# Optimization experiments

Hardware: AMD Instinct MI355X
Metric: run time of the kernel (lower is better)

Reference implementation:

```python
import jax, jax.numpy as jnp
import numpy as np

B, S, D, H = 2, 2048, 1024, 16
HD = D // H          # 64
ROT = HD // 2        # 32

def _rope(x, cos, sin):
    # x: [B,S,H,HD] -> pairs [B,S,H,ROT,2]; cos/sin: [S,ROT] -> [1,S,1,ROT]
    x2 = x.reshape(x.shape[:3] + (ROT, 2))
    x0, x1 = x2[..., 0], x2[..., 1]
    c = cos[None, :, None, :]
    s = sin[None, :, None, :]
    out = jnp.stack([x0 * c - x1 * s, x1 * c + x0 * s], axis=-1)
    return out.reshape(x.shape)

def setup_inputs() -> dict:
    key = jax.random.key(0)
    ks = jax.random.split(key, 5)
    hidden_states = jax.random.normal(ks[0], (B, S, D), dtype=jnp.float32)
    # proper rotary cos/sin table: [S, ROT, 2]
    inv_freq = 1.0 / (10000.0 ** (np.arange(0, ROT, dtype=np.float32) / ROT))
    t = np.arange(S, dtype=np.float32)
    ang = np.outer(t, inv_freq)  # [S, ROT]
    freqs = jnp.asarray(np.stack([np.cos(ang), np.sin(ang)], axis=-1), dtype=jnp.float32)
    sc = 1.0 / np.sqrt(D)
    wq = jax.random.normal(ks[1], (D, D), dtype=jnp.float32) * sc
    wk = jax.random.normal(ks[2], (D, D), dtype=jnp.float32) * sc
    wv = jax.random.normal(ks[3], (D, D), dtype=jnp.float32) * sc
    wo = jax.random.normal(ks[4], (D, D), dtype=jnp.float32) * sc
    return {"hidden_states": hidden_states, "freqs": freqs, "wq": wq, "wk": wk, "wv": wv, "wo": wo}

def reference(hidden_states, freqs, wq, wk, wv, wo):
    b, s, _ = hidden_states.shape
    scaling = HD ** -0.5
    q = (hidden_states @ wq.T).reshape(b, s, H, HD)
    k = (hidden_states @ wk.T).reshape(b, s, H, HD)
    v = (hidden_states @ wv.T).reshape(b, s, H, HD)
    cos, sin = freqs[:s, :, 0], freqs[:s, :, 1]
    q = _rope(q, cos, sin)
    k = _rope(k, cos, sin)
    # [B,H,S,S] scores, fp32 softmax
    scores = jnp.einsum('bqhd,bkhd->bhqk', q, k) * scaling
    attn = jax.nn.softmax(scores.astype(jnp.float32), axis=-1).astype(q.dtype)
    out = jnp.einsum('bhqk,bkhd->bqhd', attn, v).reshape(b, s, D)
    return out @ wo.T
```

## Files before the change

kernel.cpp:

```cpp
#include <hip/hip_runtime.h>
#include <hip/hip_bf16.h>

typedef __attribute__((ext_vector_type(8))) short bf16x8;
typedef __attribute__((ext_vector_type(4))) float f32x4;
typedef __attribute__((ext_vector_type(16))) float f32x16;
typedef __attribute__((ext_vector_type(2))) float f32x2;
typedef unsigned short u16;

#define Bc   2
#define Sc   2048
#define Dc   1024
#define Hc   16
#define HDc  64
#define ROTc 32
#define Mrows 4096

__device__ __forceinline__ u16 f2bf(float x) {
  union { float f; unsigned u; } v{x};
  unsigned r = v.u + 0x7fffu + ((v.u >> 16) & 1u);
  return (u16)(r >> 16);
}
__device__ __forceinline__ float bf2f(u16 x) {
  union { unsigned u; float f; } v{(unsigned)x << 16};
  return v.f;
}
__device__ __forceinline__ unsigned cvtpk(float a, float b) {
  unsigned r;
  asm("v_cvt_pk_bf16_f32 %0, %1, %2" : "=v"(r) : "v"(a), "v"(b));
  return r;
}
__device__ __forceinline__ f32x2 pmax2(f32x2 a, f32x2 b) {
  f32x2 r;
  r.x = fmaxf(a.x, b.x);
  r.y = fmaxf(a.y, b.y);
  return r;
}

__device__ __forceinline__ void gload_lds16(const void* g, void* l) {
  __builtin_amdgcn_global_load_lds(
      (const __attribute__((address_space(1))) void*)g,
      (__attribute__((address_space(3))) void*)l, 16, 0, 0);
}

__global__ void cvt_all(const float* __restrict__ h, const float* __restrict__ q,
                        const float* __restrict__ k, const float* __restrict__ v,
                        const float* __restrict__ o,
                        u16* __restrict__ hb, u16* __restrict__ qb, u16* __restrict__ kb,
                        u16* __restrict__ vb, u16* __restrict__ ob) {
  size_t i = ((size_t)blockIdx.x * 256 + threadIdx.x) * 4;
  const float* s;
  u16* d;
  size_t off;
  if (i < (size_t)Mrows * Dc) {
    s = h; d = hb; off = i;
  } else {
    size_t j = i - (size_t)Mrows * Dc;
    int w = (int)(j >> 20);
    off = j & ((1u << 20) - 1);
    s = (w == 0) ? q : (w == 1) ? k : (w == 2) ? v : o;
    d = (w == 0) ? qb : (w == 1) ? kb : (w == 2) ? vb : ob;
  }
  float4 val = *reinterpret_cast<const float4*>(s + off);
  u16 r0 = f2bf(val.x), r1 = f2bf(val.y), r2 = f2bf(val.z), r3 = f2bf(val.w);
  ushort4 outv = {r0, r1, r2, r3};
  *reinterpret_cast<ushort4*>(d + off) = outv;
}

__global__ void gemm_qkv(const u16* __restrict__ A, const u16* __restrict__ W0,
                         const u16* __restrict__ W1, const u16* __restrict__ W2,
                         const float* __restrict__ freqs,
                         u16* __restrict__ Qo, u16* __restrict__ Ko,
                         u16* __restrict__ Vo) {
  __shared__ u16 As[128 * 32];
  __shared__ u16 Bs[128 * 32];
  const int by = blockIdx.y;
  const int wsel = by >> 3;
  const int n0 = (by & 7) * 128;
  const int m0 = blockIdx.x * 128;
  const u16* Bm = (wsel == 0) ? W0 : (wsel == 1) ? W1 : W2;
  const int t = threadIdx.x;
  const int w = t >> 6;
  const int lane = t & 63;
  const int wm = w >> 1, wn = w & 1;
  const int c = lane & 15, g = lane >> 4;
  const int srow = t >> 2, skoff = (t & 3) * 8;

  f32x4 acc[4][4] = {};

  const u16* ag = A + (size_t)(m0 + srow) * Dc + skoff;
  const u16* bg = Bm + (size_t)(n0 + srow) * Dc + skoff;
  u16* al = &As[(w * 16) * 32];
  u16* bl = &Bs[(w * 16) * 32];

  for (int k0 = 0; k0 < Dc; k0 += 32) {
    gload_lds16(ag + k0, al);
    gload_lds16(ag + k0 + (size_t)64 * Dc, al + 64 * 32);
    gload_lds16(bg + k0, bl);
    gload_lds16(bg + k0 + (size_t)64 * Dc, bl + 64 * 32);
    __syncthreads();
    bf16x8 a[4], b[4];
#pragma unroll
    for (int f = 0; f < 4; ++f) {
      a[f] = *(const bf16x8*)&As[(wm * 64 + f * 16 + c) * 32 + g * 8];
      b[f] = *(const bf16x8*)&Bs[(wn * 64 + f * 16 + c) * 32 + g * 8];
    }
#pragma unroll
    for (int fm = 0; fm < 4; ++fm)
#pragma unroll
      for (int fn = 0; fn < 4; ++fn)
        acc[fm][fn] =
            __builtin_amdgcn_mfma_f32_16x16x32_bf16(a[fm], b[fn], acc[fm][fn], 0, 0, 0);
    __syncthreads();
  }

  u16* dst = (wsel == 0) ? Qo : (wsel == 1) ? Ko : Vo;
  const float qsc = (wsel == 0) ? 0.125f * 1.44269504f : 1.0f;
  const int codd = c & 1;
#pragma unroll
  for (int fm = 0; fm < 4; ++fm)
#pragma unroll
    for (int fn = 0; fn < 4; ++fn)
#pragma unroll
      for (int r = 0; r < 4; ++r) {
        const int m = m0 + wm * 64 + fm * 16 + g * 4 + r;
        const int n = n0 + wn * 64 + fn * 16 + c;
        float v = acc[fm][fn][r];
        const int b = m >> 11, s = m & (Sc - 1);
        const int hh = n >> 6, d = n & 63;
        size_t idx;
        if (wsel < 2) {
          const float other = __shfl_xor(v, 1);
          const float2 f = reinterpret_cast<const float2*>(freqs)[s * ROTc + (d >> 1)];
          v = codd ? (v * f.x + other * f.y) : (v * f.x - other * f.y);
          v *= qsc;
          idx = (((size_t)(b * Hc + hh) * Sc) + s) * HDc + d;
        } else {
          idx = ((size_t)(b * Hc + hh) * HDc + d) * Sc + s;
        }
        dst[idx] = f2bf(v);
      }
}

__global__ void gemm_out(const u16* __restrict__ A, const u16* __restrict__ Bm,
                         float* __restrict__ C) {
  __shared__ u16 As[64 * 32];
  __shared__ u16 Bs[128 * 32];
  const int m0 = blockIdx.x * 64;
  const int n0 = blockIdx.y * 128;
  const int t = threadIdx.x;
  const int w = t >> 6;
  const int lane = t & 63;
  const int wm = w >> 1, wn = w & 1;
  const int c = lane & 15, g = lane >> 4;
  const int srow = t >> 2, skoff = (t & 3) * 8;

  f32x4 acc[2][4] = {};

  const u16* ag = A + (size_t)(m0 + srow) * Dc + skoff;
  const u16* bg = Bm + (size_t)(n0 + srow) * Dc + skoff;
  u16* al = &As[(w * 16) * 32];
  u16* bl = &Bs[(w * 16) * 32];

  for (int k0 = 0; k0 < Dc; k0 += 32) {
    gload_lds16(ag + k0, al);
    gload_lds16(bg + k0, bl);
    gload_lds16(bg + k0 + (size_t)64 * Dc, bl + 64 * 32);
    __syncthreads();
    bf16x8 a[2], b[4];
#pragma unroll
    for (int f = 0; f < 2; ++f)
      a[f] = *(const bf16x8*)&As[(wm * 32 + f * 16 + c) * 32 + g * 8];
#pragma unroll
    for (int f = 0; f < 4; ++f)
      b[f] = *(const bf16x8*)&Bs[(wn * 64 + f * 16 + c) * 32 + g * 8];
#pragma unroll
    for (int fm = 0; fm < 2; ++fm)
#pragma unroll
      for (int fn = 0; fn < 4; ++fn)
        acc[fm][fn] =
            __builtin_amdgcn_mfma_f32_16x16x32_bf16(a[fm], b[fn], acc[fm][fn], 0, 0, 0);
    __syncthreads();
  }

#pragma unroll
  for (int fm = 0; fm < 2; ++fm)
#pragma unroll
    for (int fn = 0; fn < 4; ++fn)
#pragma unroll
      for (int r = 0; r < 4; ++r) {
        const int m = m0 + wm * 32 + fm * 16 + g * 4 + r;
        const int n = n0 + wn * 64 + fn * 16 + c;
        C[(size_t)m * Dc + n] = acc[fm][fn][r];
      }
}

__global__ __launch_bounds__(256, 2) void flash_attn(
    const u16* __restrict__ Q, const u16* __restrict__ Kb,
    const u16* __restrict__ Vt, u16* __restrict__ Ob) {
  __shared__ u16 Ks[2][32 * 128];
  __shared__ u16 Vs[2][32 * 128];
  const int orig = blockIdx.x;
  const int wg = (orig & 7) * 64 + (orig >> 3);
  const int bh = wg >> 4;
  const int q0 = (wg & 15) * 128;
  const int t = threadIdx.x, w = t >> 6, lane = t & 63;
  const int l31 = lane & 31, hi = lane >> 5;
  const int sr = t >> 4;
  const int su = (t & 15) ^ (sr & 15);
  const int skv = sr + ((su >> 3) << 5);
  const int sd8 = (su & 7) * 8;
  const int rsw = (l31 & 15);

  const u16* Qp = Q + (size_t)bh * Sc * HDc;
  const u16* Kp = Kb + (size_t)bh * Sc * HDc;
  const u16* Vp = Vt + (size_t)bh * HDc * Sc;

  const int q = q0 + w * 32 + l31;
  bf16x8 aq[4];
#pragma unroll
  for (int kd = 0; kd < 4; ++kd)
    aq[kd] = *(const bf16x8*)(Qp + (size_t)q * HDc + kd * 16 + hi * 8);

  float m_run = -1e30f, l_run = 0.f;
  f32x16 o0 = {}, o1 = {};
  bf16x8 va0[4], va1[4];

  auto STAGE = [&](int tile, int bb) {
    const int base = tile * 64;
    gload_lds16(Kp + (size_t)(base + skv) * HDc + sd8, &Ks[bb][w * 512]);
    gload_lds16(Kp + (size_t)(base + skv + 16) * HDc + sd8, &Ks[bb][2048 + w * 512]);
    gload_lds16(Vp + (size_t)skv * Sc + base + sd8, &Vs[bb][w * 512]);
    gload_lds16(Vp + (size_t)(skv + 16) * Sc + base + sd8, &Vs[bb][2048 + w * 512]);
  };
  auto QKF = [&](const u16* kbase, f32x16& S0, f32x16& S1) {
    __builtin_amdgcn_s_setprio(1);
#pragma unroll
    for (int kd = 0; kd < 4; ++kd) {
      const int u0 = kd * 2 + hi;
      bf16x8 a0 = *(const bf16x8*)&kbase[l31 * 128 + (u0 ^ rsw) * 8];
      bf16x8 a1 = *(const bf16x8*)&kbase[l31 * 128 + ((u0 + 8) ^ rsw) * 8];
      S0 = __builtin_amdgcn_mfma_f32_32x32x16_bf16(a0, aq[kd], S0, 0, 0, 0);
      S1 = __builtin_amdgcn_mfma_f32_32x32x16_bf16(a1, aq[kd], S1, 0, 0, 0);
    }
    __builtin_amdgcn_s_setprio(0);
  };
  auto LOADV = [&](const u16* vbase) {
#pragma unroll
    for (int ks = 0; ks < 4; ++ks) {
      const int uv = ks * 2 + hi;
      va0[ks] = *(const bf16x8*)&vbase[l31 * 128 + (uv ^ rsw) * 8];
      va1[ks] = *(const bf16x8*)&vbase[l31 * 128 + ((uv + 8) ^ rsw) * 8];
    }
  };
  auto SMPV = [&](f32x16& S0, f32x16& S1) {
    f32x2 t4[4];
#pragma unroll
    for (int i = 0; i < 4; ++i) {
      f32x2 e0; e0.x = S0[2 * i]; e0.y = S0[2 * i + 1];
      f32x2 e1; e1.x = S0[2 * i + 8]; e1.y = S0[2 * i + 9];
      f32x2 e2; e2.x = S1[2 * i]; e2.y = S1[2 * i + 1];
      f32x2 e3; e3.x = S1[2 * i + 8]; e3.y = S1[2 * i + 9];
      t4[i] = pmax2(pmax2(e0, e1), pmax2(e2, e3));
    }
    f32x2 tp = pmax2(pmax2(t4[0], t4[1]), pmax2(t4[2], t4[3]));
    float mt = fmaxf(tp.x, tp.y);
    mt = fmaxf(mt, __shfl_xor(mt, 32));
    const bool skip = __all(mt <= m_run + 8.0f);
    if (!skip) {
      const float mn2 = fmaxf(m_run, mt);
      const float scl = __builtin_amdgcn_exp2f(m_run - mn2);
      m_run = mn2;
      l_run *= scl;
      o0 *= scl;
      o1 *= scl;
    }
    const float mn = m_run;
#pragma unroll
    for (int r = 0; r < 16; ++r) {
      S0[r] = __builtin_amdgcn_exp2f(S0[r] - mn);
      S1[r] = __builtin_amdgcn_exp2f(S1[r] - mn);
    }
    f32x2 ac;
    ac.x = 0.f; ac.y = 0.f;
#pragma unroll
    for (int i = 0; i < 8; ++i) {
      f32x2 e0; e0.x = S0[2 * i]; e0.y = S0[2 * i + 1];
      f32x2 e1; e1.x = S1[2 * i]; e1.y = S1[2 * i + 1];
      ac += e0 + e1;
    }
    float rs = ac.x + ac.y;
    rs += __shfl_xor(rs, 32);
    l_run += rs;
    unsigned pk0[8], pk1[8];
#pragma unroll
    for (int B = 0; B < 4; ++B)
#pragma unroll
      for (int s2 = 0; s2 < 2; ++s2) {
        pk0[B * 2 + s2] = cvtpk(S0[4 * B + 2 * s2], S0[4 * B + 2 * s2 + 1]);
        pk1[B * 2 + s2] = cvtpk(S1[4 * B + 2 * s2], S1[4 * B + 2 * s2 + 1]);
      }
    bf16x8 bpv[4];
#pragma unroll
    for (int ks = 0; ks < 4; ++ks) {
      const unsigned* pk = (ks >> 1) ? pk1 : pk0;
      const int m2 = (ks & 1) * 4;
      const unsigned A0 = pk[m2 + 0], A1 = pk[m2 + 1];
      const unsigned B0 = pk[m2 + 2], B1 = pk[m2 + 3];
      const unsigned L0 = hi ? B0 : A0, L1 = hi ? B1 : A1;
      const unsigned R0 = hi ? A0 : B0, R1 = hi ? A1 : B1;
      const unsigned X0 = __shfl_xor(R0, 32), X1 = __shfl_xor(R1, 32);
      union { unsigned u[4]; bf16x8 v; } bp;
      bp.u[0] = hi ? X0 : L0;
      bp.u[1] = hi ? X1 : L1;
      bp.u[2] = hi ? L0 : X0;
      bp.u[3] = hi ? L1 : X1;
      bpv[ks] = bp.v;
    }
    __builtin_amdgcn_s_setprio(1);
#pragma unroll
    for (int ks = 0; ks < 4; ++ks) {
      o0 = __builtin_amdgcn_mfma_f32_32x32x16_bf16(va0[ks], bpv[ks], o0, 0, 0, 0);
      o1 = __builtin_amdgcn_mfma_f32_32x32x16_bf16(va1[ks], bpv[ks], o1, 0, 0, 0);
    }
    __builtin_amdgcn_s_setprio(0);
  };

  STAGE(0, 0);
  STAGE(1, 1);
  __syncthreads();
  f32x16 sp0 = {}, sp1 = {};
  QKF(&Ks[0][0], sp0, sp1);
  LOADV(&Vs[0][0]);
  __syncthreads();

  int buf = 1;
  for (int tt = 1; tt < 32; ++tt) {
    if (tt < 31) STAGE(tt + 1, buf ^ 1);
    f32x16 sn0 = {}, sn1 = {};
    QKF(&Ks[buf][0], sn0, sn1);
    SMPV(sp0, sp1);
    LOADV(&Vs[buf][0]);
    __syncthreads();
    sp0 = sn0;
    sp1 = sn1;
    buf ^= 1;
  }
  SMPV(sp0, sp1);

  const float rl = 1.0f / l_run;
  const int b = bh >> 4, hh = bh & 15;
  u16* orow = Ob + ((size_t)b * Sc + q) * Dc + hh * HDc;
#pragma unroll
  for (int B2 = 0; B2 < 4; ++B2) {
    const float v0 = o0[4 * B2 + 0] * rl, v1 = o0[4 * B2 + 1] * rl;
    const float v2 = o0[4 * B2 + 2] * rl, v3 = o0[4 * B2 + 3] * rl;
    uint2 pv;
    pv.x = cvtpk(v0, v1);
    pv.y = cvtpk(v2, v3);
    *reinterpret_cast<uint2*>(orow + 8 * B2 + 4 * hi) = pv;
  }
#pragma unroll
  for (int B2 = 0; B2 < 4; ++B2) {
    const float v0 = o1[4 * B2 + 0] * rl, v1 = o1[4 * B2 + 1] * rl;
    const float v2 = o1[4 * B2 + 2] * rl, v3 = o1[4 * B2 + 3] * rl;
    uint2 pv;
    pv.x = cvtpk(v0, v1);
    pv.y = cvtpk(v2, v3);
    *reinterpret_cast<uint2*>(orow + 32 + 8 * B2 + 4 * hi) = pv;
  }
}

extern "C" void kernel_launch(void* const* d_in, const int* in_sizes, int n_in,
                              void* d_out, int out_size, void* d_ws, size_t ws_size,
                              hipStream_t stream) {
  (void)in_sizes; (void)n_in; (void)out_size; (void)ws_size;
  const float* hidden = (const float*)d_in[0];
  const float* freqs = (const float*)d_in[1];
  const float* wq = (const float*)d_in[2];
  const float* wk = (const float*)d_in[3];
  const float* wv = (const float*)d_in[4];
  const float* wo = (const float*)d_in[5];
  float* out = (float*)d_out;

  char* ws = (char*)d_ws;
  const size_t MB8 = (size_t)Mrows * Dc * 2;
  const size_t WB = (size_t)Dc * Dc * 2;
  u16* hb = (u16*)ws;  ws += MB8;
  u16* wqb = (u16*)ws; ws += WB;
  u16* wkb = (u16*)ws; ws += WB;
  u16* wvb = (u16*)ws; ws += WB;
  u16* wob = (u16*)ws; ws += WB;
  u16* qb = (u16*)ws;  ws += MB8;
  u16* kb = (u16*)ws;  ws += MB8;
  u16* vtb = (u16*)ws; ws += MB8;
  u16* ab = (u16*)ws;  ws += MB8;

  cvt_all<<<8192, 256, 0, stream>>>(hidden, wq, wk, wv, wo, hb, wqb, wkb, wvb, wob);
  gemm_qkv<<<dim3(32, 24), 256, 0, stream>>>(hb, wqb, wkb, wvb, freqs, qb, kb, vtb);
  flash_attn<<<512, 256, 0, stream>>>(qb, kb, vtb, ab);
  gemm_out<<<dim3(64, 8), 256, 0, stream>>>(ab, wob, out);
}
```

Measured before the change: 138.5 us.

## Split KV sequence across two wave groups per flash attention block

Each attention workgroup now has 512 threads in two groups of four waves. Each group processes half of the KV sequence for the same 128 queries, in 16 tiles instead of 32, using its own double-buffered LDS region. At the end, group 1 writes its partial O, max and sum to LDS and group 0 merges them with a log-sum-exp rescale before writing. This doubles the active waves per block to shorten the serial KV loop and improve latency hiding. The cost is twice the LDS per block, 64KB, which may limit blocks per CU, plus an extra LDS reduction and syncs at the end.

Result: slower. 331.3 us (+139.3%).

```diff
diff --git a/kernel.cpp b/kernel.cpp
--- a/kernel.cpp
+++ b/kernel.cpp
@@ -194,19 +194,20 @@
       }
 }
 
-__global__ __launch_bounds__(256, 2) void flash_attn(
+__global__ __launch_bounds__(512, 4) void flash_attn(
     const u16* __restrict__ Q, const u16* __restrict__ Kb,
     const u16* __restrict__ Vt, u16* __restrict__ Ob) {
-  __shared__ u16 Ks[2][32 * 128];
-  __shared__ u16 Vs[2][32 * 128];
+  __shared__ u16 smem[32768];
   const int orig = blockIdx.x;
   const int wg = (orig & 7) * 64 + (orig >> 3);
   const int bh = wg >> 4;
   const int q0 = (wg & 15) * 128;
   const int t = threadIdx.x, w = t >> 6, lane = t & 63;
+  const int grp = w >> 2, wl = w & 3;
+  const int ts = t & 255;
   const int l31 = lane & 31, hi = lane >> 5;
-  const int sr = t >> 4;
-  const int su = (t & 15) ^ (sr & 15);
+  const int sr = ts >> 4;
+  const int su = (ts & 15) ^ (sr & 15);
   const int skv = sr + ((su >> 3) << 5);
   const int sd8 = (su & 7) * 8;
   const int rsw = (l31 & 15);
@@ -214,8 +215,10 @@
   const u16* Qp = Q + (size_t)bh * Sc * HDc;
   const u16* Kp = Kb + (size_t)bh * Sc * HDc;
   const u16* Vp = Vt + (size_t)bh * HDc * Sc;
-
-  const int q = q0 + w * 32 + l31;
+  u16* const Kg = smem + grp * 8192;
+  u16* const Vg = smem + 16384 + grp * 8192;
+
+  const int q = q0 + wl * 32 + l31;
   bf16x8 aq[4];
 #pragma unroll
   for (int kd = 0; kd < 4; ++kd)
@@ -226,11 +229,13 @@
   bf16x8 va0[4], va1[4];
 
   auto STAGE = [&](int tile, int bb) {
-    const int base = tile * 64;
-    gload_lds16(Kp + (size_t)(base + skv) * HDc + sd8, &Ks[bb][w * 512]);
-    gload_lds16(Kp + (size_t)(base + skv + 16) * HDc + sd8, &Ks[bb][2048 + w * 512]);
-    gload_lds16(Vp + (size_t)skv * Sc + base + sd8, &Vs[bb][w * 512]);
-    gload_lds16(Vp + (size_t)(skv + 16) * Sc + base + sd8, &Vs[bb][2048 + w * 512]);
+    const int base = grp * 1024 + tile * 64;
+    gload_lds16(Kp + (size_t)(base + skv) * HDc + sd8, Kg + bb * 4096 + wl * 512);
+    gload_lds16(Kp + (size_t)(base + skv + 16) * HDc + sd8,
+                Kg + bb * 4096 + 2048 + wl * 512);
+    gload_lds16(Vp + (size_t)skv * Sc + base + sd8, Vg + bb * 4096 + wl * 512);
+    gload_lds16(Vp + (size_t)(skv + 16) * Sc + base + sd8,
+                Vg + bb * 4096 + 2048 + wl * 512);
   };
   auto QKF = [&](const u16* kbase, f32x16& S0, f32x16& S1) {
     __builtin_amdgcn_s_setprio(1);
@@ -329,17 +334,17 @@
   STAGE(1, 1);
   __syncthreads();
   f32x16 sp0 = {}, sp1 = {};
-  QKF(&Ks[0][0], sp0, sp1);
-  LOADV(&Vs[0][0]);
+  QKF(Kg, sp0, sp1);
+  LOADV(Vg);
   __syncthreads();
 
   int buf = 1;
-  for (int tt = 1; tt < 32; ++tt) {
-    if (tt < 31) STAGE(tt + 1, buf ^ 1);
+  for (int tt = 1; tt < 16; ++tt) {
+    if (tt < 15) STAGE(tt + 1, buf ^ 1);
     f32x16 sn0 = {}, sn1 = {};
-    QKF(&Ks[buf][0], sn0, sn1);
+    QKF(Kg + buf * 4096, sn0, sn1);
     SMPV(sp0, sp1);
-    LOADV(&Vs[buf][0]);
+    LOADV(Vg + buf * 4096);
     __syncthreads();
     sp0 = sn0;
     sp1 = sn1;
@@ -347,26 +352,49 @@
   }
   SMPV(sp0, sp1);
 
-  const float rl = 1.0f / l_run;
-  const int b = bh >> 4, hh = bh & 15;
-  u16* orow = Ob + ((size_t)b * Sc + q) * Dc + hh * HDc;
-#pragma unroll
-  for (int B2 = 0; B2 < 4; ++B2) {
-    const float v0 = o0[4 * B2 + 0] * rl, v1 = o0[4 * B2 + 1] * rl;
-    const float v2 = o0[4 * B2 + 2] * rl, v3 = o0[4 * B2 + 3] * rl;
-    uint2 pv;
-    pv.x = cvtpk(v0, v1);
-    pv.y = cvtpk(v2, v3);
-    *reinterpret_cast<uint2*>(orow + 8 * B2 + 4 * hi) = pv;
-  }
-#pragma unroll
-  for (int B2 = 0; B2 < 4; ++B2) {
-    const float v0 = o1[4 * B2 + 0] * rl, v1 = o1[4 * B2 + 1] * rl;
-    const float v2 = o1[4 * B2 + 2] * rl, v3 = o1[4 * B2 + 3] * rl;
-    uint2 pv;
-    pv.x = cvtpk(v0, v1);
-    pv.y = cvtpk(v2, v3);
-    *reinterpret_cast<uint2*>(orow + 32 + 8 * B2 + 4 * hi) = pv;
+  float* fl = reinterpret_cast<float*>(smem);
+  const int slot = (wl * 64 + lane) * 35;
+  __syncthreads();
+  if (grp == 1) {
+#pragma unroll
+    for (int j = 0; j < 16; ++j) fl[slot + j] = o0[j];
+#pragma unroll
+    for (int j = 0; j < 16; ++j) fl[slot + 16 + j] = o1[j];
+    fl[slot + 32] = m_run;
+    fl[slot + 33] = l_run;
+  }
+  __syncthreads();
+  if (grp == 0) {
+    const float mB = fl[slot + 32], lB = fl[slot + 33];
+    const float mx = fmaxf(m_run, mB);
+    const float sA = __builtin_amdgcn_exp2f(m_run - mx);
+    const float sB = __builtin_amdgcn_exp2f(mB - mx);
+    const float rd = 1.0f / (l_run * sA + lB * sB);
+    const float cA = sA * rd, cB = sB * rd;
+    const int b = bh >> 4, hh = bh & 15;
+    u16* orow = Ob + ((size_t)b * Sc + q) * Dc + hh * HDc;
+#pragma unroll
+    for (int B2 = 0; B2 < 4; ++B2) {
+      const float v0 = o0[4 * B2 + 0] * cA + fl[slot + 4 * B2 + 0] * cB;
+      const float v1 = o0[4 * B2 + 1] * cA + fl[slot + 4 * B2 + 1] * cB;
+      const float v2 = o0[4 * B2 + 2] * cA + fl[slot + 4 * B2 + 2] * cB;
+      const float v3 = o0[4 * B2 + 3] * cA + fl[slot + 4 * B2 + 3] * cB;
+      uint2 pv;
+      pv.x = cvtpk(v0, v1);
+      pv.y = cvtpk(v2, v3);
+      *reinterpret_cast<uint2*>(orow + 8 * B2 + 4 * hi) = pv;
+    }
+#pragma unroll
+    for (int B2 = 0; B2 < 4; ++B2) {
+      const float v0 = o1[4 * B2 + 0] * cA + fl[slot + 16 + 4 * B2 + 0] * cB;
+      const float v1 = o1[4 * B2 + 1] * cA + fl[slot + 16 + 4 * B2 + 1] * cB;
+      const float v2 = o1[4 * B2 + 2] * cA + fl[slot + 16 + 4 * B2 + 2] * cB;
+      const float v3 = o1[4 * B2 + 3] * cA + fl[slot + 16 + 4 * B2 + 3] * cB;
+      uint2 pv;
+      pv.x = cvtpk(v0, v1);
+      pv.y = cvtpk(v2, v3);
+      *reinterpret_cast<uint2*>(orow + 32 + 8 * B2 + 4 * hi) = pv;
+    }
   }
 }
 
@@ -397,6 +425,6 @@
 
   cvt_all<<<8192, 256, 0, stream>>>(hidden, wq, wk, wv, wo, hb, wqb, wkb, wvb, wob);
   gemm_qkv<<<dim3(32, 24), 256, 0, stream>>>(hb, wqb, wkb, wvb, freqs, qb, kb, vtb);
-  flash_attn<<<512, 256, 0, stream>>>(qb, kb, vtb, ab);
+  flash_attn<<<512, 512, 0, stream>>>(qb, kb, vtb, ab);
   gemm_out<<<dim3(64, 8), 256, 0, stream>>>(ab, wob, out);
 }
```
